# Performance work log

Measured on AMD Instinct MI355X. Metric: run time of the kernel, lower is better.

The kernel has to match this reference:

```python
import jax, jax.numpy as jnp
import numpy as np

D_MODEL = 1024
N_HEADS = 16
HEAD_DIM = D_MODEL // N_HEADS


def setup_inputs() -> dict:
    key = jax.random.key(0)
    k_x, k_wqkv, k_bqkv, k_wout, k_bout = jax.random.split(key, 5)
    s = 1.0 / np.sqrt(D_MODEL)
    return {
        "x": jax.random.normal(k_x, (4, 2048, D_MODEL), dtype=jnp.float32),
        "W_qkv": jax.random.normal(k_wqkv, (D_MODEL, 3 * D_MODEL), dtype=jnp.float32) * s,
        "b_qkv": jax.random.normal(k_bqkv, (3 * D_MODEL,), dtype=jnp.float32) * 0.01,
        "W_out": jax.random.normal(k_wout, (D_MODEL, D_MODEL), dtype=jnp.float32) * s,
        "b_out": jax.random.normal(k_bout, (D_MODEL,), dtype=jnp.float32) * 0.01,
    }


def reference(x, W_qkv, b_qkv, W_out, b_out):
    B, T, D = x.shape
    H, Hd = N_HEADS, HEAD_DIM
    qkv = x @ W_qkv + b_qkv                          # [B,T,3D]
    qkv = qkv.reshape(B, T, 3, H, Hd)
    q, k, v = (qkv[:, :, i].transpose(0, 2, 1, 3) for i in range(3))  # [B,H,T,Hd]
    scale = 1.0 / np.sqrt(Hd)
    attn = jnp.einsum("bhqd,bhkd->bhqk", q, k) * scale  # [B,H,T,T]
    causal = jnp.tril(jnp.ones((T, T), dtype=bool))
    attn = jnp.where(causal, attn, -jnp.inf)
    attn = jax.nn.softmax(attn, axis=-1)
    out = jnp.einsum("bhqk,bhkd->bhqd", attn, v)     # [B,H,T,Hd]
    out = out.transpose(0, 2, 1, 3).reshape(B, T, D)
    return out @ W_out + b_out
```

## Files before the change

### kernel.cpp

```cpp
#include <hip/hip_runtime.h>
#include <hip/hip_bf16.h>
#include <string.h>


typedef unsigned short u16;
typedef unsigned int u32;
typedef __bf16 bf16x8 __attribute__((ext_vector_type(8)));
typedef float f32x4 __attribute__((ext_vector_type(4)));

#define MFMA16(a, b, c) __builtin_amdgcn_mfma_f32_16x16x32_bf16((a), (b), (c), 0, 0, 0)

__device__ __forceinline__ u16 f2bf(float f) {
  unsigned u = __float_as_uint(f);
  u += 0x7fffu + ((u >> 16) & 1u);
  return (u16)(u >> 16);
}

__device__ __forceinline__ u32 pk2bf(float a, float b) {
  __hip_bfloat162 h = __float22bfloat162_rn(make_float2(a, b));
  u32 r;
  memcpy(&r, &h, 4);
  return r;
}

__device__ __forceinline__ void gload_lds16(const void* g, void* l) {
  __builtin_amdgcn_global_load_lds((const __attribute__((address_space(1))) void*)g,
                                   (__attribute__((address_space(3))) void*)l, 16, 0, 0);
}

__global__ __launch_bounds__(256) void cast_x_kernel(const float* __restrict__ x,
                                                     u16* __restrict__ xb) {
  int i = blockIdx.x * 256 + threadIdx.x;
  float4 v = ((const float4*)x)[i];
  ushort4 o;
  o.x = f2bf(v.x); o.y = f2bf(v.y); o.z = f2bf(v.z); o.w = f2bf(v.w);
  ((ushort4*)xb)[i] = o;
}

__global__ __launch_bounds__(256) void tcast_kernel(const float* __restrict__ W,
                                                    u16* __restrict__ Wt, int K, int N) {
  __shared__ float tile[32][33];
  int n0 = blockIdx.x * 32, k0 = blockIdx.y * 32;
  int tx = threadIdx.x & 31, ty = threadIdx.x >> 5;
#pragma unroll
  for (int i = 0; i < 4; i++) {
    int k = ty + i * 8;
    tile[k][tx] = W[(size_t)(k0 + k) * N + n0 + tx];
  }
  __syncthreads();
#pragma unroll
  for (int i = 0; i < 4; i++) {
    int n = ty + i * 8;
    Wt[(size_t)(n0 + n) * K + k0 + tx] = f2bf(tile[tx][n]);
  }
}

__global__ __launch_bounds__(256) void gemm_qkv_kernel(const u16* __restrict__ A,
                                                       const u16* __restrict__ Bt,
                                                       const float* __restrict__ bias,
                                                       u16* __restrict__ QKV) {
  __shared__ u16 As[128 * 64];
  __shared__ u16 Bs[128 * 64];
  const int tid = threadIdx.x, w = tid >> 6, lane = tid & 63;
  const int g = lane >> 4, c = lane & 15;
  const int wr = w >> 1, wc = w & 1;
  const int m0 = blockIdx.y * 128, n0 = blockIdx.x * 128;
  const int srow = lane >> 3;
  const int sch = (lane & 7) ^ srow;
  const int cx = c & 7;

  f32x4 acc[4][4];
#pragma unroll
  for (int i = 0; i < 4; i++)
#pragma unroll
    for (int j = 0; j < 4; j++) acc[i][j] = (f32x4){0.f, 0.f, 0.f, 0.f};

  for (int k0 = 0; k0 < 1024; k0 += 64) {
    __syncthreads();
#pragma unroll
    for (int i = 0; i < 4; i++) {
      int row = w * 32 + i * 8;
      gload_lds16(A + (size_t)(m0 + row + srow) * 1024 + k0 + sch * 8,
                  (char*)As + row * 128);
      gload_lds16(Bt + (size_t)(n0 + row + srow) * 1024 + k0 + sch * 8,
                  (char*)Bs + row * 128);
    }
    __syncthreads();

#pragma unroll
    for (int kk = 0; kk < 2; kk++) {
      bf16x8 af[4], bf[4];
#pragma unroll
      for (int mt = 0; mt < 4; mt++)
        af[mt] = *(const bf16x8*)(As + (wr * 64 + mt * 16 + c) * 64 + ((kk * 4 + g) ^ cx) * 8);
#pragma unroll
      for (int nt = 0; nt < 4; nt++)
        bf[nt] = *(const bf16x8*)(Bs + (wc * 64 + nt * 16 + c) * 64 + ((kk * 4 + g) ^ cx) * 8);
#pragma unroll
      for (int mt = 0; mt < 4; mt++)
#pragma unroll
        for (int nt = 0; nt < 4; nt++) acc[mt][nt] = MFMA16(af[mt], bf[nt], acc[mt][nt]);
    }
  }

  const float qscale = (n0 < 1024) ? 0.18033688011112042f : 1.0f;
  float bn[4];
#pragma unroll
  for (int nt = 0; nt < 4; nt++) bn[nt] = bias[n0 + wc * 64 + nt * 16 + c];
#pragma unroll
  for (int mt = 0; mt < 4; mt++) {
#pragma unroll
    for (int r = 0; r < 4; r++) {
      int m = m0 + wr * 64 + mt * 16 + g * 4 + r;
      int bb = m >> 11, t = m & 2047;
#pragma unroll
      for (int nt = 0; nt < 4; nt++) {
        int n = n0 + wc * 64 + nt * 16 + c;
        int which = n >> 10, rem = n & 1023, h = rem >> 6, d = rem & 63;
        float v = (acc[mt][nt][r] + bn[nt]) * qscale;
        QKV[(size_t)which * 8388608 + (((size_t)(bb * 16 + h) * 2048 + t) * 64 + d)] = f2bf(v);
      }
    }
  }
}

__global__ __launch_bounds__(256) void vtrans_kernel(const u16* __restrict__ V,
                                                     u16* __restrict__ Vt) {
  __shared__ u16 tile[64][65];
  int bh = blockIdx.y;
  int kt = blockIdx.x;
  int t0 = kt * 64;
  int tx = threadIdx.x & 63, ty = threadIdx.x >> 6;
  const u16* src = V + ((size_t)bh * 2048 + t0) * 64;
#pragma unroll
  for (int i = 0; i < 16; i++) {
    int tr = i * 4 + ty;
    tile[tr][tx] = src[tr * 64 + tx];
  }
  __syncthreads();
  u16* dst = Vt + ((size_t)(bh * 32 + kt)) * 4096;
#pragma unroll
  for (int i = 0; i < 16; i++) {
    int d = i * 4 + ty;
    dst[d * 64 + tx] = tile[tx][d];
  }
}

__global__ __launch_bounds__(256, 2) void attn_kernel(const u16* __restrict__ Q,
                                                      const u16* __restrict__ K,
                                                      const u16* __restrict__ Vt,
                                                      u16* __restrict__ ctx) {
  const int pr = blockIdx.x;
  const int qtA = pr, qtB = 15 - pr;
  const int h = blockIdx.y, b = blockIdx.z;
  const int bh = b * 16 + h;
  const int tid = threadIdx.x, w = tid >> 6, lane = tid & 63;
  const int g = lane >> 4, c = lane & 15;

  const u16* Kg = K + (size_t)bh * 2048 * 64;
  const u16* Vg = Vt + (size_t)bh * 32 * 4096;

  __shared__ u16 Ks[2][64 * 64];
  __shared__ u16 Vs[2][64 * 64];
  __shared__ u32 Pw[4][16 * 32];
  u32* pw = Pw[w];

  const int srow = lane >> 3;
  const int schunk = (lane & 7) ^ (srow & 7);
  const int cx = c & 7;
  const int off0 = ((g ^ cx) * 8);
  const int off1 = (((g ^ cx) ^ 4) * 8);
  const int sw = cx << 2;
  const int rbase = w * 16;

  bf16x8 onesf;
#pragma unroll
  for (int i = 0; i < 8; i++) onesf[i] = (__bf16)1.0f;

  const u16* QgA = Q + ((size_t)bh * 2048 + qtA * 128) * 64;
  bf16x8 aq[2][2];
#pragma unroll
  for (int s = 0; s < 2; s++) {
    aq[s][0] = *(const bf16x8*)(QgA + (w * 32 + s * 16 + c) * 64 + g * 8);
    aq[s][1] = *(const bf16x8*)(QgA + (w * 32 + s * 16 + c) * 64 + 32 + g * 8);
  }

  {
    gload_lds16(Kg + (size_t)(rbase + srow) * 64 + schunk * 8, (char*)(Ks[0]) + rbase * 128);
    gload_lds16(Kg + (size_t)(rbase + 8 + srow) * 64 + schunk * 8, (char*)(Ks[0]) + (rbase + 8) * 128);
    gload_lds16(Vg + (size_t)(rbase + srow) * 64 + schunk * 8, (char*)(Vs[0]) + rbase * 128);
    gload_lds16(Vg + (size_t)(rbase + 8 + srow) * 64 + schunk * 8, (char*)(Vs[0]) + (rbase + 8) * 128);
  }
  __syncthreads();

  f32x4 o[2][4], la[2];
#pragma unroll
  for (int s = 0; s < 2; s++) {
#pragma unroll
    for (int nt = 0; nt < 4; nt++) o[s][nt] = (f32x4){0.f, 0.f, 0.f, 0.f};
    la[s] = (f32x4){0.f, 0.f, 0.f, 0.f};
  }

  const int nA = 2 * qtA + 2;

  auto store_strip = [&](int qbase, int s) {
    float inv = 1.f / la[s][0];
    int q = qbase + w * 32 + s * 16 + c;
    size_t base = ((size_t)(b * 2048 + q)) * 1024 + h * 64;
#pragma unroll
    for (int nt = 0; nt < 4; nt++) {
      u32 lo = pk2bf(o[s][nt][0] * inv, o[s][nt][1] * inv);
      u32 hi = pk2bf(o[s][nt][2] * inv, o[s][nt][3] * inv);
      *(uint2*)(ctx + base + nt * 16 + g * 4) = make_uint2(lo, hi);
    }
  };

  for (int r = 0; r < 34; r++) {
    if (r) __syncthreads();

    if (r < 33) {
      const int ktn = (r + 1 < nA) ? (r + 1) : (r + 1 - nA);
      const int nb = (r + 1) & 1;
      gload_lds16(Kg + (size_t)ktn * 4096 + (size_t)(rbase + srow) * 64 + schunk * 8,
                  (char*)(Ks[nb]) + rbase * 128);
      gload_lds16(Kg + (size_t)ktn * 4096 + (size_t)(rbase + 8 + srow) * 64 + schunk * 8,
                  (char*)(Ks[nb]) + (rbase + 8) * 128);
      gload_lds16(Vg + (size_t)ktn * 4096 + (size_t)(rbase + srow) * 64 + schunk * 8,
                  (char*)(Vs[nb]) + rbase * 128);
      gload_lds16(Vg + (size_t)ktn * 4096 + (size_t)(rbase + 8 + srow) * 64 + schunk * 8,
                  (char*)(Vs[nb]) + (rbase + 8) * 128);
    }

    const bool inA = (r < nA);
    const int kt = inA ? r : (r - nA);
    const int qbase = inA ? qtA * 128 : qtB * 128;
    const int kb = kt * 64;
    const u16* Kb = Ks[r & 1];
    const u16* Vb = Vs[r & 1];

#pragma unroll
    for (int s = 0; s < 2; s++) {
      const int sbs = qbase + w * 32 + s * 16;
      if (kb <= sbs + 15) {
        f32x4 sa[4];
#pragma unroll
        for (int nt = 0; nt < 4; nt++) {
          bf16x8 k0 = *(const bf16x8*)(Kb + (nt * 16 + c) * 64 + off0);
          bf16x8 k1 = *(const bf16x8*)(Kb + (nt * 16 + c) * 64 + off1);
          f32x4 z = (f32x4){0.f, 0.f, 0.f, 0.f};
          z = MFMA16(k0, aq[s][0], z);
          z = MFMA16(k1, aq[s][1], z);
          sa[nt] = z;
        }

        const bool domask = (kb + 63 > sbs);
        float pe[4][4];
#pragma unroll
        for (int nt = 0; nt < 4; nt++)
#pragma unroll
          for (int rr = 0; rr < 4; rr++) {
            float t = sa[nt][rr];
            if (domask && (kb + nt * 16 + g * 4 + rr) > (sbs + c)) t = -1e30f;
            pe[nt][rr] = __builtin_amdgcn_exp2f(t);
          }
#pragma unroll
        for (int nt = 0; nt < 4; nt++) {
          u32 lo = pk2bf(pe[nt][0], pe[nt][1]);
          u32 hi = pk2bf(pe[nt][2], pe[nt][3]);
          *(uint2*)(pw + c * 32 + ((nt * 8 + g * 2) ^ sw)) = make_uint2(lo, hi);
        }
        bf16x8 pB0 = *(const bf16x8*)(pw + c * 32 + ((g * 4) ^ sw));
        bf16x8 pB1 = *(const bf16x8*)(pw + c * 32 + ((16 + g * 4) ^ sw));

        la[s] = MFMA16(onesf, pB0, la[s]);
        la[s] = MFMA16(onesf, pB1, la[s]);

#pragma unroll
        for (int nt = 0; nt < 4; nt++) {
          bf16x8 v0 = *(const bf16x8*)(Vb + (nt * 16 + c) * 64 + off0);
          bf16x8 v1 = *(const bf16x8*)(Vb + (nt * 16 + c) * 64 + off1);
          o[s][nt] = MFMA16(v0, pB0, o[s][nt]);
          o[s][nt] = MFMA16(v1, pB1, o[s][nt]);
        }
      }
    }

    if (r == nA - 1) {
      store_strip(qtA * 128, 0);
      store_strip(qtA * 128, 1);
#pragma unroll
      for (int s = 0; s < 2; s++) {
#pragma unroll
        for (int nt = 0; nt < 4; nt++) o[s][nt] = (f32x4){0.f, 0.f, 0.f, 0.f};
        la[s] = (f32x4){0.f, 0.f, 0.f, 0.f};
      }
      const u16* QgB = Q + ((size_t)bh * 2048 + qtB * 128) * 64;
#pragma unroll
      for (int s = 0; s < 2; s++) {
        aq[s][0] = *(const bf16x8*)(QgB + (w * 32 + s * 16 + c) * 64 + g * 8);
        aq[s][1] = *(const bf16x8*)(QgB + (w * 32 + s * 16 + c) * 64 + 32 + g * 8);
      }
    }
  }

  store_strip(qtB * 128, 0);
  store_strip(qtB * 128, 1);
}

__global__ __launch_bounds__(256) void gemm_proj_kernel(const u16* __restrict__ A,
                                                        const u16* __restrict__ Bt,
                                                        const float* __restrict__ bias,
                                                        float* __restrict__ out) {
  __shared__ u16 As[128 * 64];
  __shared__ u16 Bs[128 * 64];
  const int tid = threadIdx.x, w = tid >> 6, lane = tid & 63;
  const int g = lane >> 4, c = lane & 15;
  const int wr = w >> 1, wc = w & 1;
  const int m0 = blockIdx.y * 128, n0 = blockIdx.x * 128;
  const int srow = lane >> 3;
  const int sch = (lane & 7) ^ srow;
  const int cx = c & 7;

  f32x4 acc[4][4];
#pragma unroll
  for (int i = 0; i < 4; i++)
#pragma unroll
    for (int j = 0; j < 4; j++) acc[i][j] = (f32x4){0.f, 0.f, 0.f, 0.f};

  for (int k0 = 0; k0 < 1024; k0 += 64) {
    __syncthreads();
#pragma unroll
    for (int i = 0; i < 4; i++) {
      int row = w * 32 + i * 8;
      gload_lds16(A + (size_t)(m0 + row + srow) * 1024 + k0 + sch * 8,
                  (char*)As + row * 128);
      gload_lds16(Bt + (size_t)(n0 + row + srow) * 1024 + k0 + sch * 8,
                  (char*)Bs + row * 128);
    }
    __syncthreads();

#pragma unroll
    for (int kk = 0; kk < 2; kk++) {
      bf16x8 af[4], bf[4];
#pragma unroll
      for (int mt = 0; mt < 4; mt++)
        af[mt] = *(const bf16x8*)(As + (wr * 64 + mt * 16 + c) * 64 + ((kk * 4 + g) ^ cx) * 8);
#pragma unroll
      for (int nt = 0; nt < 4; nt++)
        bf[nt] = *(const bf16x8*)(Bs + (wc * 64 + nt * 16 + c) * 64 + ((kk * 4 + g) ^ cx) * 8);
#pragma unroll
      for (int mt = 0; mt < 4; mt++)
#pragma unroll
        for (int nt = 0; nt < 4; nt++) acc[mt][nt] = MFMA16(af[mt], bf[nt], acc[mt][nt]);
    }
  }

  float bn[4];
#pragma unroll
  for (int nt = 0; nt < 4; nt++) bn[nt] = bias[n0 + wc * 64 + nt * 16 + c];
#pragma unroll
  for (int mt = 0; mt < 4; mt++)
#pragma unroll
    for (int r = 0; r < 4; r++) {
      int m = m0 + wr * 64 + mt * 16 + g * 4 + r;
#pragma unroll
      for (int nt = 0; nt < 4; nt++) {
        int n = n0 + wc * 64 + nt * 16 + c;
        out[(size_t)m * 1024 + n] = acc[mt][nt][r] + bn[nt];
      }
    }
}

extern "C" void kernel_launch(void* const* d_in, const int* in_sizes, int n_in,
                              void* d_out, int out_size, void* d_ws, size_t ws_size,
                              hipStream_t stream) {
  const float* x = (const float*)d_in[0];
  const float* Wqkv = (const float*)d_in[1];
  const float* bqkv = (const float*)d_in[2];
  const float* Wout = (const float*)d_in[3];
  const float* bout = (const float*)d_in[4];
  float* out = (float*)d_out;

  char* ws = (char*)d_ws;
  u16* xb  = (u16*)(ws);
  u16* wqt = (u16*)(ws + 16777216);
  u16* wot = (u16*)(ws + 23068672);
  u16* Qb  = (u16*)(ws + 25165824);
  u16* Kb  = Qb + 8388608;
  u16* Vb  = Kb + 8388608;
  u16* Vt  = (u16*)(ws + 75497472);
  u16* ctx = (u16*)(ws + 92274688);

  cast_x_kernel<<<8192, 256, 0, stream>>>(x, xb);
  tcast_kernel<<<dim3(96, 32), 256, 0, stream>>>(Wqkv, wqt, 1024, 3072);
  tcast_kernel<<<dim3(32, 32), 256, 0, stream>>>(Wout, wot, 1024, 1024);
  gemm_qkv_kernel<<<dim3(24, 64), 256, 0, stream>>>(xb, wqt, bqkv, Qb);
  vtrans_kernel<<<dim3(32, 64), 256, 0, stream>>>(Vb, Vt);
  attn_kernel<<<dim3(8, 16, 4), 256, 0, stream>>>(Qb, Kb, Vt, ctx);
  gemm_proj_kernel<<<dim3(8, 64), 256, 0, stream>>>(ctx, wot, bout, out);
}
```

Measured before the change: 270.1 us.

## Fuse prep casts, write V transposed from QKV GEMM, simplify attention tiling

The three cast/transpose kernels are merged into one prep kernel, and the separate V-transpose kernel is removed by having the QKV GEMM epilogue write V directly in the transposed tile layout. The attention kernel drops its paired-tile scheme for one query tile per block, with twice as many blocks ordered longest-first. Both row strips now share the K fragment loads and V reads within one loop iteration. This cuts launches and one pass over V, but the transposed V stores from the GEMM are strided and uncoalesced, and per-block work becomes unbalanced.

Result: slower. 331.4 us (+22.7%).

```diff
diff --git a/kernel.cpp b/kernel.cpp
--- a/kernel.cpp
+++ b/kernel.cpp
@@ -28,19 +28,29 @@
                                    (__attribute__((address_space(3))) void*)l, 16, 0, 0);
 }
 
-__global__ __launch_bounds__(256) void cast_x_kernel(const float* __restrict__ x,
-                                                     u16* __restrict__ xb) {
-  int i = blockIdx.x * 256 + threadIdx.x;
-  float4 v = ((const float4*)x)[i];
-  ushort4 o;
-  o.x = f2bf(v.x); o.y = f2bf(v.y); o.z = f2bf(v.z); o.w = f2bf(v.w);
-  ((ushort4*)xb)[i] = o;
-}
-
-__global__ __launch_bounds__(256) void tcast_kernel(const float* __restrict__ W,
-                                                    u16* __restrict__ Wt, int K, int N) {
+__global__ __launch_bounds__(256) void prep_kernel(const float* __restrict__ x,
+                                                   u16* __restrict__ xb,
+                                                   const float* __restrict__ Wqkv,
+                                                   u16* __restrict__ wqt,
+                                                   const float* __restrict__ Wout,
+                                                   u16* __restrict__ wot) {
+  const int id = blockIdx.x;
+  if (id < 8192) {
+    int i = id * 256 + threadIdx.x;
+    float4 v = ((const float4*)x)[i];
+    ushort4 o;
+    o.x = f2bf(v.x); o.y = f2bf(v.y); o.z = f2bf(v.z); o.w = f2bf(v.w);
+    ((ushort4*)xb)[i] = o;
+    return;
+  }
   __shared__ float tile[32][33];
-  int n0 = blockIdx.x * 32, k0 = blockIdx.y * 32;
+  const float* W; u16* Wt; int N, n0, k0;
+  const int K = 1024;
+  if (id < 11264) {
+    int t = id - 8192;  W = Wqkv; Wt = wqt; N = 3072; n0 = (t % 96) * 32; k0 = (t / 96) * 32;
+  } else {
+    int t = id - 11264; W = Wout; Wt = wot; N = 1024; n0 = (t % 32) * 32; k0 = (t / 32) * 32;
+  }
   int tx = threadIdx.x & 31, ty = threadIdx.x >> 5;
 #pragma unroll
   for (int i = 0; i < 4; i++) {
@@ -58,7 +68,8 @@
 __global__ __launch_bounds__(256) void gemm_qkv_kernel(const u16* __restrict__ A,
                                                        const u16* __restrict__ Bt,
                                                        const float* __restrict__ bias,
-                                                       u16* __restrict__ QKV) {
+                                                       u16* __restrict__ QKV,
+                                                       u16* __restrict__ Vt) {
   __shared__ u16 As[128 * 64];
   __shared__ u16 Bs[128 * 64];
   const int tid = threadIdx.x, w = tid >> 6, lane = tid & 63;
@@ -103,7 +114,8 @@
     }
   }
 
-  const float qscale = (n0 < 1024) ? 0.18033688011112042f : 1.0f;
+  const int which = n0 >> 10;
+  const float qscale = (which == 0) ? 0.18033688011112042f : 1.0f;
   float bn[4];
 #pragma unroll
   for (int nt = 0; nt < 4; nt++) bn[nt] = bias[n0 + wc * 64 + nt * 16 + c];
@@ -116,33 +128,15 @@
 #pragma unroll
       for (int nt = 0; nt < 4; nt++) {
         int n = n0 + wc * 64 + nt * 16 + c;
-        int which = n >> 10, rem = n & 1023, h = rem >> 6, d = rem & 63;
-        float v = (acc[mt][nt][r] + bn[nt]) * qscale;
-        QKV[(size_t)which * 8388608 + (((size_t)(bb * 16 + h) * 2048 + t) * 64 + d)] = f2bf(v);
-      }
-    }
-  }
-}
-
-__global__ __launch_bounds__(256) void vtrans_kernel(const u16* __restrict__ V,
-                                                     u16* __restrict__ Vt) {
-  __shared__ u16 tile[64][65];
-  int bh = blockIdx.y;
-  int kt = blockIdx.x;
-  int t0 = kt * 64;
-  int tx = threadIdx.x & 63, ty = threadIdx.x >> 6;
-  const u16* src = V + ((size_t)bh * 2048 + t0) * 64;
-#pragma unroll
-  for (int i = 0; i < 16; i++) {
-    int tr = i * 4 + ty;
-    tile[tr][tx] = src[tr * 64 + tx];
-  }
-  __syncthreads();
-  u16* dst = Vt + ((size_t)(bh * 32 + kt)) * 4096;
-#pragma unroll
-  for (int i = 0; i < 16; i++) {
-    int d = i * 4 + ty;
-    dst[d * 64 + tx] = tile[tx][d];
+        int rem = n & 1023, h = rem >> 6, d = rem & 63;
+        u16 val = f2bf((acc[mt][nt][r] + bn[nt]) * qscale);
+        if (which == 2) {
+          Vt[((size_t)(bb * 16 + h) * 32 + (t >> 6)) * 4096 + (size_t)d * 64 + (t & 63)] = val;
+        } else {
+          QKV[(size_t)which * 8388608 + (((size_t)(bb * 16 + h) * 2048 + t) * 64 + d)] = val;
+        }
+      }
+    }
   }
 }
 
@@ -150,8 +144,7 @@
                                                       const u16* __restrict__ K,
                                                       const u16* __restrict__ Vt,
                                                       u16* __restrict__ ctx) {
-  const int pr = blockIdx.x;
-  const int qtA = pr, qtB = 15 - pr;
+  const int qt = 15 - blockIdx.x;
   const int h = blockIdx.y, b = blockIdx.z;
   const int bh = b * 16 + h;
   const int tid = threadIdx.x, w = tid >> 6, lane = tid & 63;
@@ -177,20 +170,18 @@
 #pragma unroll
   for (int i = 0; i < 8; i++) onesf[i] = (__bf16)1.0f;
 
-  const u16* QgA = Q + ((size_t)bh * 2048 + qtA * 128) * 64;
+  const u16* Qg = Q + ((size_t)bh * 2048 + qt * 128) * 64;
   bf16x8 aq[2][2];
 #pragma unroll
   for (int s = 0; s < 2; s++) {
-    aq[s][0] = *(const bf16x8*)(QgA + (w * 32 + s * 16 + c) * 64 + g * 8);
-    aq[s][1] = *(const bf16x8*)(QgA + (w * 32 + s * 16 + c) * 64 + 32 + g * 8);
-  }
-
-  {
-    gload_lds16(Kg + (size_t)(rbase + srow) * 64 + schunk * 8, (char*)(Ks[0]) + rbase * 128);
-    gload_lds16(Kg + (size_t)(rbase + 8 + srow) * 64 + schunk * 8, (char*)(Ks[0]) + (rbase + 8) * 128);
-    gload_lds16(Vg + (size_t)(rbase + srow) * 64 + schunk * 8, (char*)(Vs[0]) + rbase * 128);
-    gload_lds16(Vg + (size_t)(rbase + 8 + srow) * 64 + schunk * 8, (char*)(Vs[0]) + (rbase + 8) * 128);
-  }
+    aq[s][0] = *(const bf16x8*)(Qg + (w * 32 + s * 16 + c) * 64 + g * 8);
+    aq[s][1] = *(const bf16x8*)(Qg + (w * 32 + s * 16 + c) * 64 + 32 + g * 8);
+  }
+
+  gload_lds16(Kg + (size_t)(rbase + srow) * 64 + schunk * 8, (char*)(Ks[0]) + rbase * 128);
+  gload_lds16(Kg + (size_t)(rbase + 8 + srow) * 64 + schunk * 8, (char*)(Ks[0]) + (rbase + 8) * 128);
+  gload_lds16(Vg + (size_t)(rbase + srow) * 64 + schunk * 8, (char*)(Vs[0]) + rbase * 128);
+  gload_lds16(Vg + (size_t)(rbase + 8 + srow) * 64 + schunk * 8, (char*)(Vs[0]) + (rbase + 8) * 128);
   __syncthreads();
 
   f32x4 o[2][4], la[2];
@@ -201,11 +192,32 @@
     la[s] = (f32x4){0.f, 0.f, 0.f, 0.f};
   }
 
-  const int nA = 2 * qtA + 2;
-
-  auto store_strip = [&](int qbase, int s) {
+  const int nR = 2 * qt + 2;
+
+  auto softmax = [&](const f32x4 (&sa)[4], int kb, int sbs, bf16x8& p0, bf16x8& p1) {
+    const bool domask = (kb + 63 > sbs);
+    float pe[4][4];
+#pragma unroll
+    for (int nt = 0; nt < 4; nt++)
+#pragma unroll
+      for (int rr = 0; rr < 4; rr++) {
+        float t = sa[nt][rr];
+        if (domask && (kb + nt * 16 + g * 4 + rr) > (sbs + c)) t = -1e30f;
+        pe[nt][rr] = __builtin_amdgcn_exp2f(t);
+      }
+#pragma unroll
+    for (int nt = 0; nt < 4; nt++) {
+      u32 lo = pk2bf(pe[nt][0], pe[nt][1]);
+      u32 hi = pk2bf(pe[nt][2], pe[nt][3]);
+      *(uint2*)(pw + c * 32 + ((nt * 8 + g * 2) ^ sw)) = make_uint2(lo, hi);
+    }
+    p0 = *(const bf16x8*)(pw + c * 32 + ((g * 4) ^ sw));
+    p1 = *(const bf16x8*)(pw + c * 32 + ((16 + g * 4) ^ sw));
+  };
+
+  auto store_strip = [&](int s) {
     float inv = 1.f / la[s][0];
-    int q = qbase + w * 32 + s * 16 + c;
+    int q = qt * 128 + w * 32 + s * 16 + c;
     size_t base = ((size_t)(b * 2048 + q)) * 1024 + h * 64;
 #pragma unroll
     for (int nt = 0; nt < 4; nt++) {
@@ -215,96 +227,73 @@
     }
   };
 
-  for (int r = 0; r < 34; r++) {
+  for (int r = 0; r < nR; r++) {
     if (r) __syncthreads();
 
-    if (r < 33) {
-      const int ktn = (r + 1 < nA) ? (r + 1) : (r + 1 - nA);
+    if (r + 1 < nR) {
       const int nb = (r + 1) & 1;
-      gload_lds16(Kg + (size_t)ktn * 4096 + (size_t)(rbase + srow) * 64 + schunk * 8,
+      const size_t tb = (size_t)(r + 1) * 4096;
+      gload_lds16(Kg + tb + (size_t)(rbase + srow) * 64 + schunk * 8,
                   (char*)(Ks[nb]) + rbase * 128);
-      gload_lds16(Kg + (size_t)ktn * 4096 + (size_t)(rbase + 8 + srow) * 64 + schunk * 8,
+      gload_lds16(Kg + tb + (size_t)(rbase + 8 + srow) * 64 + schunk * 8,
                   (char*)(Ks[nb]) + (rbase + 8) * 128);
-      gload_lds16(Vg + (size_t)ktn * 4096 + (size_t)(rbase + srow) * 64 + schunk * 8,
+      gload_lds16(Vg + tb + (size_t)(rbase + srow) * 64 + schunk * 8,
                   (char*)(Vs[nb]) + rbase * 128);
-      gload_lds16(Vg + (size_t)ktn * 4096 + (size_t)(rbase + 8 + srow) * 64 + schunk * 8,
+      gload_lds16(Vg + tb + (size_t)(rbase + 8 + srow) * 64 + schunk * 8,
                   (char*)(Vs[nb]) + (rbase + 8) * 128);
     }
 
-    const bool inA = (r < nA);
-    const int kt = inA ? r : (r - nA);
-    const int qbase = inA ? qtA * 128 : qtB * 128;
-    const int kb = kt * 64;
+    const int kb = r * 64;
+    const int sb0 = qt * 128 + w * 32;
+    const bool l1 = kb <= sb0 + 31;
+    const bool l0 = kb <= sb0 + 15;
     const u16* Kb = Ks[r & 1];
     const u16* Vb = Vs[r & 1];
 
-#pragma unroll
-    for (int s = 0; s < 2; s++) {
-      const int sbs = qbase + w * 32 + s * 16;
-      if (kb <= sbs + 15) {
-        f32x4 sa[4];
-#pragma unroll
-        for (int nt = 0; nt < 4; nt++) {
-          bf16x8 k0 = *(const bf16x8*)(Kb + (nt * 16 + c) * 64 + off0);
-          bf16x8 k1 = *(const bf16x8*)(Kb + (nt * 16 + c) * 64 + off1);
-          f32x4 z = (f32x4){0.f, 0.f, 0.f, 0.f};
-          z = MFMA16(k0, aq[s][0], z);
-          z = MFMA16(k1, aq[s][1], z);
-          sa[nt] = z;
+    if (l1) {
+      f32x4 sa1[4], sa0[4];
+#pragma unroll
+      for (int nt = 0; nt < 4; nt++) {
+        bf16x8 k0 = *(const bf16x8*)(Kb + (nt * 16 + c) * 64 + off0);
+        bf16x8 k1 = *(const bf16x8*)(Kb + (nt * 16 + c) * 64 + off1);
+        f32x4 z = (f32x4){0.f, 0.f, 0.f, 0.f};
+        z = MFMA16(k0, aq[1][0], z);
+        z = MFMA16(k1, aq[1][1], z);
+        sa1[nt] = z;
+        if (l0) {
+          f32x4 y = (f32x4){0.f, 0.f, 0.f, 0.f};
+          y = MFMA16(k0, aq[0][0], y);
+          y = MFMA16(k1, aq[0][1], y);
+          sa0[nt] = y;
         }
-
-        const bool domask = (kb + 63 > sbs);
-        float pe[4][4];
-#pragma unroll
-        for (int nt = 0; nt < 4; nt++)
-#pragma unroll
-          for (int rr = 0; rr < 4; rr++) {
-            float t = sa[nt][rr];
-            if (domask && (kb + nt * 16 + g * 4 + rr) > (sbs + c)) t = -1e30f;
-            pe[nt][rr] = __builtin_amdgcn_exp2f(t);
-          }
-#pragma unroll
-        for (int nt = 0; nt < 4; nt++) {
-          u32 lo = pk2bf(pe[nt][0], pe[nt][1]);
-          u32 hi = pk2bf(pe[nt][2], pe[nt][3]);
-          *(uint2*)(pw + c * 32 + ((nt * 8 + g * 2) ^ sw)) = make_uint2(lo, hi);
+      }
+
+      bf16x8 p10, p11, p00, p01;
+      softmax(sa1, kb, sb0 + 16, p10, p11);
+      la[1] = MFMA16(onesf, p10, la[1]);
+      la[1] = MFMA16(onesf, p11, la[1]);
+      if (l0) {
+        softmax(sa0, kb, sb0, p00, p01);
+        la[0] = MFMA16(onesf, p00, la[0]);
+        la[0] = MFMA16(onesf, p01, la[0]);
+      }
+
+#pragma unroll
+      for (int nt = 0; nt < 4; nt++) {
+        bf16x8 v0 = *(const bf16x8*)(Vb + (nt * 16 + c) * 64 + off0);
+        bf16x8 v1 = *(const bf16x8*)(Vb + (nt * 16 + c) * 64 + off1);
+        o[1][nt] = MFMA16(v0, p10, o[1][nt]);
+        o[1][nt] = MFMA16(v1, p11, o[1][nt]);
+        if (l0) {
+          o[0][nt] = MFMA16(v0, p00, o[0][nt]);
+          o[0][nt] = MFMA16(v1, p01, o[0][nt]);
         }
-        bf16x8 pB0 = *(const bf16x8*)(pw + c * 32 + ((g * 4) ^ sw));
-        bf16x8 pB1 = *(const bf16x8*)(pw + c * 32 + ((16 + g * 4) ^ sw));
-
-        la[s] = MFMA16(onesf, pB0, la[s]);
-        la[s] = MFMA16(onesf, pB1, la[s]);
-
-#pragma unroll
-        for (int nt = 0; nt < 4; nt++) {
-          bf16x8 v0 = *(const bf16x8*)(Vb + (nt * 16 + c) * 64 + off0);
-          bf16x8 v1 = *(const bf16x8*)(Vb + (nt * 16 + c) * 64 + off1);
-          o[s][nt] = MFMA16(v0, pB0, o[s][nt]);
-          o[s][nt] = MFMA16(v1, pB1, o[s][nt]);
-        }
-      }
-    }
-
-    if (r == nA - 1) {
-      store_strip(qtA * 128, 0);
-      store_strip(qtA * 128, 1);
-#pragma unroll
-      for (int s = 0; s < 2; s++) {
-#pragma unroll
-        for (int nt = 0; nt < 4; nt++) o[s][nt] = (f32x4){0.f, 0.f, 0.f, 0.f};
-        la[s] = (f32x4){0.f, 0.f, 0.f, 0.f};
-      }
-      const u16* QgB = Q + ((size_t)bh * 2048 + qtB * 128) * 64;
-#pragma unroll
-      for (int s = 0; s < 2; s++) {
-        aq[s][0] = *(const bf16x8*)(QgB + (w * 32 + s * 16 + c) * 64 + g * 8);
-        aq[s][1] = *(const bf16x8*)(QgB + (w * 32 + s * 16 + c) * 64 + 32 + g * 8);
-      }
-    }
-  }
-
-  store_strip(qtB * 128, 0);
-  store_strip(qtB * 128, 1);
+      }
+    }
+  }
+
+  store_strip(0);
+  store_strip(1);
 }
 
 __global__ __launch_bounds__(256) void gemm_proj_kernel(const u16* __restrict__ A,
@@ -387,15 +376,11 @@
   u16* wot = (u16*)(ws + 23068672);
   u16* Qb  = (u16*)(ws + 25165824);
   u16* Kb  = Qb + 8388608;
-  u16* Vb  = Kb + 8388608;
   u16* Vt  = (u16*)(ws + 75497472);
   u16* ctx = (u16*)(ws + 92274688);
 
-  cast_x_kernel<<<8192, 256, 0, stream>>>(x, xb);
-  tcast_kernel<<<dim3(96, 32), 256, 0, stream>>>(Wqkv, wqt, 1024, 3072);
-  tcast_kernel<<<dim3(32, 32), 256, 0, stream>>>(Wout, wot, 1024, 1024);
-  gemm_qkv_kernel<<<dim3(24, 64), 256, 0, stream>>>(xb, wqt, bqkv, Qb);
-  vtrans_kernel<<<dim3(32, 64), 256, 0, stream>>>(Vb, Vt);
-  attn_kernel<<<dim3(8, 16, 4), 256, 0, stream>>>(Qb, Kb, Vt, ctx);
+  prep_kernel<<<12288, 256, 0, stream>>>(x, xb, Wqkv, wqt, Wout, wot);
+  gemm_qkv_kernel<<<dim3(24, 64), 256, 0, stream>>>(xb, wqt, bqkv, Qb, Vt);
+  attn_kernel<<<dim3(16, 16, 4), 256, 0, stream>>>(Qb, Kb, Vt, ctx);
   gemm_proj_kernel<<<dim3(8, 64), 256, 0, stream>>>(ctx, wot, bout, out);
 }
```
